# Performance work log

Measured on AMD Instinct MI355X. Metric: run time of the kernel, lower is better.

Reference implementation:

```python
import jax, jax.numpy as jnp
import numpy as np

H = 16  # heads

def setup_inputs() -> dict:
    key = jax.random.key(0)
    k1, k2, k3 = jax.random.split(key, 3)
    B, N, D = 2, 2048, 1024
    x = jax.random.normal(k1, (B, N, D), dtype=jnp.float32)
    W1 = jax.random.normal(k2, (D, 3 * D), dtype=jnp.float32) * (1.0 / np.sqrt(D))
    b1 = jnp.zeros((3 * D,), dtype=jnp.float32)
    W2 = jax.random.normal(k3, (D, D), dtype=jnp.float32) * (1.0 / np.sqrt(D))
    b2 = jnp.zeros((D,), dtype=jnp.float32)
    return {"x": x, "W1": W1, "b1": b1, "W2": W2, "b2": b2}

def reference(x, W1, b1, W2, b2):
    B, N, D = x.shape
    Dh = D // H  # head dim
    qkv = x @ W1 + b1                         # [B,N,3D]
    q, k, v = jnp.split(qkv, 3, axis=-1)
    q = q.reshape(B, N, H, Dh).transpose(0, 2, 1, 3)  # [B,H,N,Dh]
    k = k.reshape(B, N, H, Dh).transpose(0, 2, 1, 3)
    v = v.reshape(B, N, H, Dh).transpose(0, 2, 1, 3)
    scale = 1.0 / np.sqrt(Dh)
    w = jnp.einsum('bhnd,bhmd->bhnm', q, k) * scale   # [B,H,N,N]
    w = jax.nn.softmax(w, axis=-1)
    out = jnp.einsum('bhnm,bhmd->bhnd', w, v)         # [B,H,N,Dh]
    out = out.transpose(0, 2, 1, 3).reshape(B, N, D)
    return out @ W2 + b2
```

## Files before the change

kernel.cpp:

```cpp
#include <hip/hip_runtime.h>
#include <hip/hip_bf16.h>
#include <stdint.h>

#define B_   2
#define H_   16
#define N_   2048
#define D_   1024
#define DH   64
#define MTOK 4096

#define LOG2E 1.44269504088896f

typedef __attribute__((ext_vector_type(8)))  short bf16x8;
typedef __attribute__((ext_vector_type(4)))  float f32x4;
typedef __attribute__((ext_vector_type(16))) float f32x16;
typedef __attribute__((ext_vector_type(2)))  unsigned u32x2;
typedef __attribute__((ext_vector_type(4)))  unsigned short us4;

#define VMCNT_ASM(N) asm volatile("s_waitcnt vmcnt(" #N ")" ::: "memory")

static __device__ __forceinline__ unsigned short f2bf(float f) {
    union { float f; unsigned u; } v; v.f = f;
    unsigned r = v.u + 0x7fffu + ((v.u >> 16) & 1u);
    return (unsigned short)(r >> 16);
}

static __device__ __forceinline__ unsigned f2u(float x) {
    union { float f; unsigned u; } v; v.f = x; return v.u;
}
static __device__ __forceinline__ float u2f(unsigned x) {
    union { unsigned u; float f; } v; v.u = x; return v.f;
}

static __device__ __forceinline__ unsigned cvt_pk_bf16(float lo, float hi) {
    unsigned r;
    asm("v_cvt_pk_bf16_f32 %0, %1, %2" : "=v"(r) : "v"(lo), "v"(hi));
    return r;
}

static __device__ __forceinline__ bf16x8 frag_from_u32(unsigned a, unsigned b, unsigned c, unsigned d) {
    union { unsigned u[4]; bf16x8 v; } x;
    x.u[0] = a; x.u[1] = b; x.u[2] = c; x.u[3] = d;
    return x.v;
}

static __device__ __forceinline__ void load_lds16(const void* g, void* l) {
    __builtin_amdgcn_global_load_lds(
        (const __attribute__((address_space(1))) unsigned int*)g,
        (__attribute__((address_space(3))) unsigned int*)l, 16, 0, 0);
}

__global__ __launch_bounds__(256) void k_pre(const float* __restrict__ x,
                                             unsigned short* __restrict__ xb,
                                             const float* __restrict__ W1,
                                             unsigned short* __restrict__ w1t,
                                             const float* __restrict__ W2,
                                             unsigned short* __restrict__ w2t) {
    int blk = blockIdx.x;
    int t = threadIdx.x;
    if (blk < 4096) {
        int idx = (blk * 256 + t) * 4;
        float4 v = *(const float4*)(x + idx);
        us4 o;
        o.x = f2bf(v.x); o.y = f2bf(v.y); o.z = f2bf(v.z); o.w = f2bf(v.w);
        *(us4*)(xb + idx) = o;
        return;
    }
    const float* in;
    unsigned short* out;
    int C, bx, by;
    if (blk < 4864) { in = W1; out = w1t; C = 3072; int b2 = blk - 4096; bx = b2 % 48; by = b2 / 48; }
    else            { in = W2; out = w2t; C = 1024; int b2 = blk - 4864; bx = b2 % 16; by = b2 / 16; }
    const int R = 1024;
    __shared__ float tile[64][65];
    int c0 = bx * 64, r0 = by * 64;
    int tr = t >> 4, tc = (t & 15) * 4;
#pragma unroll
    for (int p = 0; p < 4; p++) {
        int row = p * 16 + tr;
        float4 v = *(const float4*)(in + (size_t)(r0 + row) * C + c0 + tc);
        tile[row][tc + 0] = v.x; tile[row][tc + 1] = v.y;
        tile[row][tc + 2] = v.z; tile[row][tc + 3] = v.w;
    }
    __syncthreads();
    int oc = t >> 4, orr = (t & 15) * 4;
#pragma unroll
    for (int p = 0; p < 4; p++) {
        int crow = p * 16 + oc;
        us4 o;
        o.x = f2bf(tile[orr + 0][crow]);
        o.y = f2bf(tile[orr + 1][crow]);
        o.z = f2bf(tile[orr + 2][crow]);
        o.w = f2bf(tile[orr + 3][crow]);
        *(us4*)(out + (size_t)(c0 + crow) * R + r0 + orr) = o;
    }
}

__global__ __launch_bounds__(512, 2) void k_gemm0(const unsigned short* __restrict__ A,
                                                  const unsigned short* __restrict__ Bt,
                                                  const float* __restrict__ bias,
                                                  unsigned short* __restrict__ qdst,
                                                  unsigned short* __restrict__ kdst,
                                                  unsigned short* __restrict__ vdst) {
    __shared__ unsigned short lds[57344];
    const int K = 1024, NT = 16;
    int tid = threadIdx.x;
    int lane = tid & 63, wv = tid >> 6;
    int wm = wv >> 2, wn = wv & 3;
    int F = blockIdx.x;
    int L = (F & 7) * 32 + (F >> 3);
    int n0 = (L % 16) * 192;
    int m0 = (L / 16) * 256;

    f32x4 acc[8][3];
#pragma unroll
    for (int i = 0; i < 8; i++)
#pragma unroll
        for (int j = 0; j < 3; j++) {
            f32x4 z; z[0] = 0.f; z[1] = 0.f; z[2] = 0.f; z[3] = 0.f;
            acc[i][j] = z;
        }

    auto stage = [&](int t) {
        int p = t & 1;
        int k0 = t * 64;
        unsigned short* ab = &lds[p * 16384];
        unsigned short* bb = &lds[32768 + p * 12288];
#pragma unroll
        for (int i = 0; i < 4; i++) {
            int u = i * 512 + tid;
            int r = u >> 3, c8 = u & 7;
            int c8s = c8 ^ (r & 7);
            int db = (i * 512 + wv * 64) * 8;
            load_lds16(A + (size_t)(m0 + r) * K + k0 + c8s * 8, &ab[db]);
            if (i < 3)
                load_lds16(Bt + (size_t)(n0 + r) * K + k0 + c8s * 8, &bb[db]);
        }
    };

    stage(0);
    stage(1);

    const int ml = lane & 15, ul = lane >> 4;
    bf16x8 afr[8], bfr[3];

#pragma unroll 1
    for (int t = 0; t < NT; ++t) {
        if (t < NT - 1) { VMCNT_ASM(7); }
        else            { VMCNT_ASM(0); }
        __builtin_amdgcn_s_barrier();

        const unsigned short* ab = &lds[(t & 1) * 16384];
        const unsigned short* bb = &lds[32768 + (t & 1) * 12288];

#pragma unroll
        for (int kk = 0; kk < 2; ++kk) {
            int ck = ((kk * 4 + ul) ^ (ml & 7)) * 8;
#pragma unroll
            for (int nj = 0; nj < 3; nj++)
                bfr[nj] = *(const bf16x8*)&bb[(wn * 48 + nj * 16 + ml) * 64 + ck];
#pragma unroll
            for (int q = 0; q < 8; q++)
                afr[q] = *(const bf16x8*)&ab[(wm * 128 + q * 16 + ml) * 64 + ck];
            __builtin_amdgcn_s_barrier();
            __builtin_amdgcn_s_setprio(1);
#pragma unroll
            for (int q = 0; q < 8; q++)
#pragma unroll
                for (int nj = 0; nj < 3; nj++)
                    acc[q][nj] = __builtin_amdgcn_mfma_f32_16x16x32_bf16(
                        afr[q], bfr[nj], acc[q][nj], 0, 0, 0);
            __builtin_amdgcn_s_setprio(0);
            __builtin_amdgcn_s_barrier();
        }
        if (t + 2 < NT) stage(t + 2);
    }

#pragma unroll
    for (int nj = 0; nj < 3; nj++) {
        int col = n0 + wn * 48 + nj * 16 + (lane & 15);
        float bv = bias[col];
        int which = col >> 10;
        int hd = (col >> 6) & 15;
        int dh = col & 63;
        float scl = (which == 0) ? (0.125f * LOG2E) : 1.0f;
#pragma unroll
        for (int mi = 0; mi < 8; mi++) {
            int rbase = m0 + wm * 128 + mi * 16 + (lane >> 4) * 4;
#pragma unroll
            for (int r = 0; r < 4; r++) {
                int tok = rbase + r;
                int bb2 = tok >> 11, nn = tok & 2047;
                float vvv = (acc[mi][nj][r] + bv) * scl;
                size_t chunk = ((size_t)(bb2 * H_ + hd) * 64 + (nn >> 5)) * 2048;
                if (which == 0) {
                    qdst[((size_t)(bb2 * H_ + hd) * N_ + nn) * DH + dh] = f2bf(vvv);
                } else if (which == 1) {
                    int lane2 = ((dh >> 3) & 1) * 32 + (nn & 31);
                    kdst[chunk + (dh >> 4) * 512 + lane2 * 8 + (dh & 7)] = f2bf(vvv);
                } else {
                    int lane2 = ((nn >> 3) & 1) * 32 + (dh & 31);
                    int islot = (dh >> 5) * 2 + ((nn >> 4) & 1);
                    vdst[chunk + islot * 512 + lane2 * 8 + (nn & 7)] = f2bf(vvv);
                }
            }
        }
    }
}

__global__ __launch_bounds__(512, 2) void k_gemm1(const unsigned short* __restrict__ A,
                                                  const unsigned short* __restrict__ Bt,
                                                  const float* __restrict__ bias,
                                                  float* __restrict__ outp) {
    __shared__ unsigned short lds1[32768];
    const int K = 1024, NT = 16;
    int tid = threadIdx.x;
    int lane = tid & 63, wv = tid >> 6;
    int wm = wv >> 2, wn = wv & 3;
    int F = blockIdx.x;
    int L = (F & 7) * 32 + (F >> 3);
    int n0 = (L % 8) * 128;
    int m0 = (L / 8) * 128;
    int bIdx = m0 >> 11;
    int ntok0 = m0 & 2047;

    f32x4 acc[4][2];
#pragma unroll
    for (int i = 0; i < 4; i++)
#pragma unroll
        for (int j = 0; j < 2; j++) {
            f32x4 z; z[0] = 0.f; z[1] = 0.f; z[2] = 0.f; z[3] = 0.f;
            acc[i][j] = z;
        }

    auto stage = [&](int t) {
        int p = t & 1;
        const unsigned short* aptr = A + ((size_t)(bIdx * H_ + t) * N_ + ntok0) * DH;
        const unsigned short* bptr = Bt + (size_t)n0 * K + t * 64;
        unsigned short* ab = &lds1[p * 8192];
        unsigned short* bb = &lds1[16384 + p * 8192];
#pragma unroll
        for (int i = 0; i < 2; i++) {
            int u = i * 512 + tid;
            int r = u >> 3, c8 = u & 7;
            int c8s = c8 ^ (r & 7);
            int db = (i * 512 + wv * 64) * 8;
            load_lds16(aptr + (size_t)r * DH + c8s * 8, &ab[db]);
            load_lds16(bptr + (size_t)r * K  + c8s * 8, &bb[db]);
        }
    };

    stage(0);
    stage(1);

    const int ml = lane & 15, ul = lane >> 4;
    bf16x8 afr[4], bfr[2];

#pragma unroll 1
    for (int t = 0; t < NT; ++t) {
        if (t < NT - 1) { VMCNT_ASM(4); }
        else            { VMCNT_ASM(0); }
        __builtin_amdgcn_s_barrier();

        const unsigned short* ab = &lds1[(t & 1) * 8192];
        const unsigned short* bb = &lds1[16384 + (t & 1) * 8192];

#pragma unroll
        for (int kk = 0; kk < 2; ++kk) {
            int ck = ((kk * 4 + ul) ^ (ml & 7)) * 8;
#pragma unroll
            for (int nj = 0; nj < 2; nj++)
                bfr[nj] = *(const bf16x8*)&bb[(wn * 32 + nj * 16 + ml) * 64 + ck];
#pragma unroll
            for (int q = 0; q < 4; q++)
                afr[q] = *(const bf16x8*)&ab[(wm * 64 + q * 16 + ml) * 64 + ck];
            __builtin_amdgcn_s_barrier();
            __builtin_amdgcn_s_setprio(1);
#pragma unroll
            for (int q = 0; q < 4; q++)
#pragma unroll
                for (int nj = 0; nj < 2; nj++)
                    acc[q][nj] = __builtin_amdgcn_mfma_f32_16x16x32_bf16(
                        afr[q], bfr[nj], acc[q][nj], 0, 0, 0);
            __builtin_amdgcn_s_setprio(0);
            __builtin_amdgcn_s_barrier();
        }
        if (t + 2 < NT) stage(t + 2);
    }

#pragma unroll
    for (int nj = 0; nj < 2; nj++) {
        int col = n0 + wn * 32 + nj * 16 + ml;
        float bv = bias[col];
#pragma unroll
        for (int mi = 0; mi < 4; mi++) {
            int rbase = m0 + wm * 64 + mi * 16 + (lane >> 4) * 4;
#pragma unroll
            for (int r = 0; r < 4; r++)
                outp[(size_t)(rbase + r) * D_ + col] = acc[mi][nj][r] + bv;
        }
    }
}

__global__ __launch_bounds__(512, 2) void k_attn(const unsigned short* __restrict__ qh,
                                                 const unsigned short* __restrict__ ks,
                                                 const unsigned short* __restrict__ vs,
                                                 unsigned short* __restrict__ o) {
    __shared__ unsigned short smem[40960];
    unsigned short* kb = smem;
    unsigned short* vb = smem + 16384;
    float* red = (float*)smem;

    int tid = threadIdx.x;
    int lane = tid & 63, wv = tid >> 6;
    int qsub = wv >> 1;
    int kvh  = wv & 1;
    int F = blockIdx.x;
    int L = (F & 7) * 64 + (F >> 3);
    int bh = L >> 4;
    int q0 = (L & 15) * 128 + qsub * 32;
    int ln = lane & 31, hi = lane >> 5;
    const size_t bhO = (size_t)bh * N_ * DH;

    const unsigned short* qp = qh + bhO;
    bf16x8 qf[4];
#pragma unroll
    for (int kk = 0; kk < 4; kk++)
        qf[kk] = *(const bf16x8*)(qp + (size_t)(q0 + ln) * DH + kk * 16 + hi * 8);

    const unsigned short* kg = ks + (size_t)bh * 131072;
    const unsigned short* vg = vs + (size_t)bh * 131072;

    int sbuf = wv >> 1;
    int sl   = wv & 1;
    int sh   = sbuf & 1;
    const unsigned short* srcb = ((sbuf >> 1) ? vg : kg) + (size_t)sh * 65536 + sl * 2048;
    auto stageT = [&](int kr, int vr, int t) {
        unsigned short* dstb = (sbuf >> 1)
            ? vb + (vr * 2 + sh) * 4096 + sl * 2048
            : kb + (kr * 2 + sh) * 4096 + sl * 2048;
#pragma unroll
        for (int i = 0; i < 4; i++)
            load_lds16(srcb + (size_t)t * 4096 + i * 512 + lane * 8, dstb + i * 512);
    };

    f32x16 o0, o1, ZEROV;
#pragma unroll
    for (int r = 0; r < 16; r++) { o0[r] = 0.f; o1[r] = 0.f; ZEROV[r] = 0.f; }
    float m = -INFINITY, l = 0.f;

    auto softmax_pv = [&](const f32x16& sa, const f32x16& sb, const unsigned short* vB) {
        float mx[8];
#pragma unroll
        for (int i = 0; i < 8; i++)
            mx[i] = fmaxf(fmaxf(sa[i], sa[i + 8]), fmaxf(sb[i], sb[i + 8]));
#pragma unroll
        for (int i = 0; i < 4; i++) mx[i] = fmaxf(mx[i], mx[i + 4]);
        float mt = fmaxf(fmaxf(mx[0], mx[2]), fmaxf(mx[1], mx[3]));
        {
            u32x2 sw = __builtin_amdgcn_permlane32_swap(f2u(mt), f2u(mt), false, false);
            mt = fmaxf(u2f(sw[0]), u2f(sw[1]));
        }
        if (!__all(mt <= m + 8.0f)) {
            float mn = fmaxf(m, mt);
            float fs = __builtin_amdgcn_exp2f(m - mn);
            m = mn;
            l *= fs;
#pragma unroll
            for (int r = 0; r < 16; r++) { o0[r] *= fs; o1[r] *= fs; }
        }
        float pa[16], pb[16];
#pragma unroll
        for (int r = 0; r < 16; r++) {
            pa[r] = __builtin_amdgcn_exp2f(sa[r] - m);
            pb[r] = __builtin_amdgcn_exp2f(sb[r] - m);
        }
        float sm[8];
#pragma unroll
        for (int i = 0; i < 8; i++) sm[i] = (pa[i] + pa[i + 8]) + (pb[i] + pb[i + 8]);
#pragma unroll
        for (int i = 0; i < 4; i++) sm[i] = sm[i] + sm[i + 4];
        float sum = (sm[0] + sm[2]) + (sm[1] + sm[3]);
        {
            u32x2 sw = __builtin_amdgcn_permlane32_swap(f2u(sum), f2u(sum), false, false);
            sum = u2f(sw[0]) + u2f(sw[1]);
        }
        l += sum;

        unsigned pka[8], pkb[8];
#pragma unroll
        for (int i = 0; i < 8; i++) {
            pka[i] = cvt_pk_bf16(pa[2 * i], pa[2 * i + 1]);
            pkb[i] = cvt_pk_bf16(pb[2 * i], pb[2 * i + 1]);
        }
        u32x2 s0 = __builtin_amdgcn_permlane32_swap(pka[0], pka[2], false, false);
        u32x2 s1 = __builtin_amdgcn_permlane32_swap(pka[1], pka[3], false, false);
        u32x2 s2 = __builtin_amdgcn_permlane32_swap(pka[4], pka[6], false, false);
        u32x2 s3 = __builtin_amdgcn_permlane32_swap(pka[5], pka[7], false, false);
        bf16x8 pf0 = frag_from_u32(s0[0], s1[0], s0[1], s1[1]);
        bf16x8 pf1 = frag_from_u32(s2[0], s3[0], s2[1], s3[1]);
        s0 = __builtin_amdgcn_permlane32_swap(pkb[0], pkb[2], false, false);
        s1 = __builtin_amdgcn_permlane32_swap(pkb[1], pkb[3], false, false);
        s2 = __builtin_amdgcn_permlane32_swap(pkb[4], pkb[6], false, false);
        s3 = __builtin_amdgcn_permlane32_swap(pkb[5], pkb[7], false, false);
        bf16x8 pf2 = frag_from_u32(s0[0], s1[0], s0[1], s1[1]);
        bf16x8 pf3 = frag_from_u32(s2[0], s3[0], s2[1], s3[1]);

        bf16x8 vf0, vf1, vf2, vf3;
        vf0 = *(const bf16x8*)&vB[0 * 512 + lane * 8];
        vf1 = *(const bf16x8*)&vB[1 * 512 + lane * 8];
        vf2 = *(const bf16x8*)&vB[2048 + 0 * 512 + lane * 8];
        vf3 = *(const bf16x8*)&vB[2048 + 1 * 512 + lane * 8];
        o0 = __builtin_amdgcn_mfma_f32_32x32x16_bf16(vf0, pf0, o0, 0, 0, 0);
        o0 = __builtin_amdgcn_mfma_f32_32x32x16_bf16(vf1, pf1, o0, 0, 0, 0);
        o0 = __builtin_amdgcn_mfma_f32_32x32x16_bf16(vf2, pf2, o0, 0, 0, 0);
        o0 = __builtin_amdgcn_mfma_f32_32x32x16_bf16(vf3, pf3, o0, 0, 0, 0);
        vf0 = *(const bf16x8*)&vB[2 * 512 + lane * 8];
        vf1 = *(const bf16x8*)&vB[3 * 512 + lane * 8];
        vf2 = *(const bf16x8*)&vB[2048 + 2 * 512 + lane * 8];
        vf3 = *(const bf16x8*)&vB[2048 + 3 * 512 + lane * 8];
        o1 = __builtin_amdgcn_mfma_f32_32x32x16_bf16(vf0, pf0, o1, 0, 0, 0);
        o1 = __builtin_amdgcn_mfma_f32_32x32x16_bf16(vf1, pf1, o1, 0, 0, 0);
        o1 = __builtin_amdgcn_mfma_f32_32x32x16_bf16(vf2, pf2, o1, 0, 0, 0);
        o1 = __builtin_amdgcn_mfma_f32_32x32x16_bf16(vf3, pf3, o1, 0, 0, 0);
    };

    stageT(0, 0, 0);
    __syncthreads();

    f32x16 sa, sb;
#pragma unroll 1
    for (int t = 0; t < 16; ++t) {
        if (t < 15) stageT((t + 1) & 1, (t + 1) % 3, t + 1);

        if (t > 0) softmax_pv(sa, sb, vb + (((t - 1) % 3) * 2 + kvh) * 4096);

        const unsigned short* kB = kb + ((t & 1) * 2 + kvh) * 4096;
        bf16x8 kfa[4], kfb[4];
#pragma unroll
        for (int i = 0; i < 4; i++) {
            kfa[i] = *(const bf16x8*)&kB[i * 512 + lane * 8];
            kfb[i] = *(const bf16x8*)&kB[2048 + i * 512 + lane * 8];
        }
        sa = __builtin_amdgcn_mfma_f32_32x32x16_bf16(kfa[0], qf[0], ZEROV, 0, 0, 0);
#pragma unroll
        for (int i = 1; i < 4; i++)
            sa = __builtin_amdgcn_mfma_f32_32x32x16_bf16(kfa[i], qf[i], sa, 0, 0, 0);
        sb = __builtin_amdgcn_mfma_f32_32x32x16_bf16(kfb[0], qf[0], ZEROV, 0, 0, 0);
#pragma unroll
        for (int i = 1; i < 4; i++)
            sb = __builtin_amdgcn_mfma_f32_32x32x16_bf16(kfb[i], qf[i], sb, 0, 0, 0);

        __syncthreads();
    }
    softmax_pv(sa, sb, vb + (0 * 2 + kvh) * 4096);
    __syncthreads();

    if (kvh == 1) {
        float* rp = red + (qsub * 64 + lane) * 34;
#pragma unroll
        for (int r = 0; r < 16; r++) { rp[r] = o0[r]; rp[16 + r] = o1[r]; }
        rp[32] = m;
        rp[33] = l;
    }
    __syncthreads();
    if (kvh == 0) {
        const float* rp = red + (qsub * 64 + lane) * 34;
        float mb = rp[32], lb = rp[33];
        float mn = fmaxf(m, mb);
        float fa = __builtin_amdgcn_exp2f(m - mn);
        float fb = __builtin_amdgcn_exp2f(mb - mn);
        float inv = 1.0f / (l * fa + lb * fb);
        float ga = fa * inv, gb = fb * inv;
        unsigned short* ob = o + bhO + (size_t)(q0 + ln) * DH;
#pragma unroll
        for (int t2 = 0; t2 < 2; t2++) {
#pragma unroll
            for (int g = 0; g < 4; g++) {
                int d = t2 * 32 + g * 8 + hi * 4;
                int rb = g * 4;
                float a0 = (t2 ? o1[rb + 0] : o0[rb + 0]) * ga + rp[t2 * 16 + rb + 0] * gb;
                float a1 = (t2 ? o1[rb + 1] : o0[rb + 1]) * ga + rp[t2 * 16 + rb + 1] * gb;
                float a2 = (t2 ? o1[rb + 2] : o0[rb + 2]) * ga + rp[t2 * 16 + rb + 2] * gb;
                float a3 = (t2 ? o1[rb + 3] : o0[rb + 3]) * ga + rp[t2 * 16 + rb + 3] * gb;
                us4 w;
                w.x = f2bf(a0); w.y = f2bf(a1); w.z = f2bf(a2); w.w = f2bf(a3);
                *(us4*)(ob + d) = w;
            }
        }
    }
}

extern "C" void kernel_launch(void* const* d_in, const int* in_sizes, int n_in,
                              void* d_out, int out_size, void* d_ws, size_t ws_size,
                              hipStream_t stream) {
    const float* x  = (const float*)d_in[0];
    const float* W1 = (const float*)d_in[1];
    const float* b1 = (const float*)d_in[2];
    const float* W2 = (const float*)d_in[3];
    const float* b2 = (const float*)d_in[4];
    float* out = (float*)d_out;

    char* ws = (char*)d_ws;
    unsigned short* xb   = (unsigned short*)(ws);
    unsigned short* w1t  = (unsigned short*)(ws + 8388608);
    unsigned short* w2t  = (unsigned short*)(ws + 14680064);
    unsigned short* qh   = (unsigned short*)(ws + 16777216);
    unsigned short* ks   = (unsigned short*)(ws + 25165824);
    unsigned short* vsb  = (unsigned short*)(ws + 33554432);
    unsigned short* attn = (unsigned short*)(ws + 41943040);

    k_pre<<<5120, 256, 0, stream>>>(x, xb, W1, w1t, W2, w2t);
    k_gemm0<<<256, 512, 0, stream>>>(xb, w1t, b1, qh, ks, vsb);
    k_attn<<<512, 512, 0, stream>>>(qh, ks, vsb, attn);
    k_gemm1<<<256, 512, 0, stream>>>(attn, w2t, b2, out);
}
```

Before: 110.1 us.

## Halve attention block to 4 waves, each wave handling two 32-row query tiles

The attention kernel now launches 256 threads per block, and each wave processes 64 query rows as two 32-row tiles. Each K/V fragment read from LDS is reused across both tiles, halving LDS traffic per unit of MFMA work. The one-tile-lagged softmax/PV software pipeline and the three-slot V ring are replaced by a simple double-buffered loop that runs QK, softmax and PV in the same iteration, with 8 loads per staging thread. Register pressure roughly doubles for the accumulators, and fewer waves per block may reduce latency hiding.

```diff
diff --git a/kernel.cpp b/kernel.cpp
--- a/kernel.cpp
+++ b/kernel.cpp
@@ -302,11 +302,11 @@
     }
 }
 
-__global__ __launch_bounds__(512, 2) void k_attn(const unsigned short* __restrict__ qh,
+__global__ __launch_bounds__(256, 2) void k_attn(const unsigned short* __restrict__ qh,
                                                  const unsigned short* __restrict__ ks,
                                                  const unsigned short* __restrict__ vs,
                                                  unsigned short* __restrict__ o) {
-    __shared__ unsigned short smem[40960];
+    __shared__ unsigned short smem[32768];
     unsigned short* kb = smem;
     unsigned short* vb = smem + 16384;
     float* red = (float*)smem;
@@ -318,38 +318,38 @@
     int F = blockIdx.x;
     int L = (F & 7) * 64 + (F >> 3);
     int bh = L >> 4;
-    int q0 = (L & 15) * 128 + qsub * 32;
+    int q0 = (L & 15) * 128 + qsub * 64;
     int ln = lane & 31, hi = lane >> 5;
     const size_t bhO = (size_t)bh * N_ * DH;
 
     const unsigned short* qp = qh + bhO;
-    bf16x8 qf[4];
-#pragma unroll
-    for (int kk = 0; kk < 4; kk++)
-        qf[kk] = *(const bf16x8*)(qp + (size_t)(q0 + ln) * DH + kk * 16 + hi * 8);
+    bf16x8 qf0[4], qf1[4];
+#pragma unroll
+    for (int kk = 0; kk < 4; kk++) {
+        qf0[kk] = *(const bf16x8*)(qp + (size_t)(q0 + ln) * DH + kk * 16 + hi * 8);
+        qf1[kk] = *(const bf16x8*)(qp + (size_t)(q0 + 32 + ln) * DH + kk * 16 + hi * 8);
+    }
 
     const unsigned short* kg = ks + (size_t)bh * 131072;
     const unsigned short* vg = vs + (size_t)bh * 131072;
 
-    int sbuf = wv >> 1;
-    int sl   = wv & 1;
-    int sh   = sbuf & 1;
-    const unsigned short* srcb = ((sbuf >> 1) ? vg : kg) + (size_t)sh * 65536 + sl * 2048;
-    auto stageT = [&](int kr, int vr, int t) {
-        unsigned short* dstb = (sbuf >> 1)
-            ? vb + (vr * 2 + sh) * 4096 + sl * 2048
-            : kb + (kr * 2 + sh) * 4096 + sl * 2048;
-#pragma unroll
-        for (int i = 0; i < 4; i++)
-            load_lds16(srcb + (size_t)t * 4096 + i * 512 + lane * 8, dstb + i * 512);
+    int sh = wv & 1;
+    unsigned short* dstb = ((wv >> 1) ? vb : kb) + sh * 8192;
+    const unsigned short* srcb = ((wv >> 1) ? vg : kg) + (size_t)sh * 65536;
+    auto stageT = [&](int ring, int t) {
+#pragma unroll
+        for (int i = 0; i < 8; i++)
+            load_lds16(srcb + (size_t)t * 4096 + i * 512 + lane * 8,
+                       dstb + ring * 4096 + i * 512);
     };
 
-    f32x16 o0, o1, ZEROV;
-#pragma unroll
-    for (int r = 0; r < 16; r++) { o0[r] = 0.f; o1[r] = 0.f; ZEROV[r] = 0.f; }
-    float m = -INFINITY, l = 0.f;
-
-    auto softmax_pv = [&](const f32x16& sa, const f32x16& sb, const unsigned short* vB) {
+    f32x16 o00, o01, o10, o11;
+#pragma unroll
+    for (int r = 0; r < 16; r++) { o00[r] = 0.f; o01[r] = 0.f; o10[r] = 0.f; o11[r] = 0.f; }
+    float m0v = -INFINITY, l0v = 0.f, m1v = -INFINITY, l1v = 0.f;
+
+    auto smax = [&](const f32x16& sa, const f32x16& sb, float& m, float& l,
+                    f32x16& oA, f32x16& oB, bf16x8* pf) {
         float mx[8];
 #pragma unroll
         for (int i = 0; i < 8; i++)
@@ -367,7 +367,7 @@
             m = mn;
             l *= fs;
 #pragma unroll
-            for (int r = 0; r < 16; r++) { o0[r] *= fs; o1[r] *= fs; }
+            for (int r = 0; r < 16; r++) { oA[r] *= fs; oB[r] *= fs; }
         }
         float pa[16], pb[16];
 #pragma unroll
@@ -397,95 +397,120 @@
         u32x2 s1 = __builtin_amdgcn_permlane32_swap(pka[1], pka[3], false, false);
         u32x2 s2 = __builtin_amdgcn_permlane32_swap(pka[4], pka[6], false, false);
         u32x2 s3 = __builtin_amdgcn_permlane32_swap(pka[5], pka[7], false, false);
-        bf16x8 pf0 = frag_from_u32(s0[0], s1[0], s0[1], s1[1]);
-        bf16x8 pf1 = frag_from_u32(s2[0], s3[0], s2[1], s3[1]);
+        pf[0] = frag_from_u32(s0[0], s1[0], s0[1], s1[1]);
+        pf[1] = frag_from_u32(s2[0], s3[0], s2[1], s3[1]);
         s0 = __builtin_amdgcn_permlane32_swap(pkb[0], pkb[2], false, false);
         s1 = __builtin_amdgcn_permlane32_swap(pkb[1], pkb[3], false, false);
         s2 = __builtin_amdgcn_permlane32_swap(pkb[4], pkb[6], false, false);
         s3 = __builtin_amdgcn_permlane32_swap(pkb[5], pkb[7], false, false);
-        bf16x8 pf2 = frag_from_u32(s0[0], s1[0], s0[1], s1[1]);
-        bf16x8 pf3 = frag_from_u32(s2[0], s3[0], s2[1], s3[1]);
-
-        bf16x8 vf0, vf1, vf2, vf3;
-        vf0 = *(const bf16x8*)&vB[0 * 512 + lane * 8];
-        vf1 = *(const bf16x8*)&vB[1 * 512 + lane * 8];
-        vf2 = *(const bf16x8*)&vB[2048 + 0 * 512 + lane * 8];
-        vf3 = *(const bf16x8*)&vB[2048 + 1 * 512 + lane * 8];
-        o0 = __builtin_amdgcn_mfma_f32_32x32x16_bf16(vf0, pf0, o0, 0, 0, 0);
-        o0 = __builtin_amdgcn_mfma_f32_32x32x16_bf16(vf1, pf1, o0, 0, 0, 0);
-        o0 = __builtin_amdgcn_mfma_f32_32x32x16_bf16(vf2, pf2, o0, 0, 0, 0);
-        o0 = __builtin_amdgcn_mfma_f32_32x32x16_bf16(vf3, pf3, o0, 0, 0, 0);
+        pf[2] = frag_from_u32(s0[0], s1[0], s0[1], s1[1]);
+        pf[3] = frag_from_u32(s2[0], s3[0], s2[1], s3[1]);
+    };
+
+    stageT(0, 0);
+    __syncthreads();
+
+#pragma unroll 1
+    for (int t = 0; t < 16; ++t) {
+        int b = t & 1;
+        if (t < 15) stageT(b ^ 1, t + 1);
+
+        const unsigned short* kB = kb + kvh * 8192 + b * 4096;
+        const unsigned short* vB = vb + kvh * 8192 + b * 4096;
+
+        bf16x8 kfa[4], kfb[4];
+#pragma unroll
+        for (int i = 0; i < 4; i++) {
+            kfa[i] = *(const bf16x8*)&kB[i * 512 + lane * 8];
+            kfb[i] = *(const bf16x8*)&kB[2048 + i * 512 + lane * 8];
+        }
+        f32x16 sa0, sb0, sa1, sb1;
+#pragma unroll
+        for (int r = 0; r < 16; r++) { sa0[r] = 0.f; sb0[r] = 0.f; sa1[r] = 0.f; sb1[r] = 0.f; }
+#pragma unroll
+        for (int i = 0; i < 4; i++) {
+            sa0 = __builtin_amdgcn_mfma_f32_32x32x16_bf16(kfa[i], qf0[i], sa0, 0, 0, 0);
+            sa1 = __builtin_amdgcn_mfma_f32_32x32x16_bf16(kfa[i], qf1[i], sa1, 0, 0, 0);
+        }
+#pragma unroll
+        for (int i = 0; i < 4; i++) {
+            sb0 = __builtin_amdgcn_mfma_f32_32x32x16_bf16(kfb[i], qf0[i], sb0, 0, 0, 0);
+            sb1 = __builtin_amdgcn_mfma_f32_32x32x16_bf16(kfb[i], qf1[i], sb1, 0, 0, 0);
+        }
+
+        bf16x8 pf0[4], pf1[4];
+        smax(sa0, sb0, m0v, l0v, o00, o01, pf0);
+        smax(sa1, sb1, m1v, l1v, o10, o11, pf1);
+
+        bf16x8 vf0 = *(const bf16x8*)&vB[0 * 512 + lane * 8];
+        bf16x8 vf1 = *(const bf16x8*)&vB[1 * 512 + lane * 8];
+        bf16x8 vf2 = *(const bf16x8*)&vB[2048 + 0 * 512 + lane * 8];
+        bf16x8 vf3 = *(const bf16x8*)&vB[2048 + 1 * 512 + lane * 8];
+        o00 = __builtin_amdgcn_mfma_f32_32x32x16_bf16(vf0, pf0[0], o00, 0, 0, 0);
+        o10 = __builtin_amdgcn_mfma_f32_32x32x16_bf16(vf0, pf1[0], o10, 0, 0, 0);
+        o00 = __builtin_amdgcn_mfma_f32_32x32x16_bf16(vf1, pf0[1], o00, 0, 0, 0);
+        o10 = __builtin_amdgcn_mfma_f32_32x32x16_bf16(vf1, pf1[1], o10, 0, 0, 0);
+        o00 = __builtin_amdgcn_mfma_f32_32x32x16_bf16(vf2, pf0[2], o00, 0, 0, 0);
+        o10 = __builtin_amdgcn_mfma_f32_32x32x16_bf16(vf2, pf1[2], o10, 0, 0, 0);
+        o00 = __builtin_amdgcn_mfma_f32_32x32x16_bf16(vf3, pf0[3], o00, 0, 0, 0);
+        o10 = __builtin_amdgcn_mfma_f32_32x32x16_bf16(vf3, pf1[3], o10, 0, 0, 0);
         vf0 = *(const bf16x8*)&vB[2 * 512 + lane * 8];
         vf1 = *(const bf16x8*)&vB[3 * 512 + lane * 8];
         vf2 = *(const bf16x8*)&vB[2048 + 2 * 512 + lane * 8];
         vf3 = *(const bf16x8*)&vB[2048 + 3 * 512 + lane * 8];
-        o1 = __builtin_amdgcn_mfma_f32_32x32x16_bf16(vf0, pf0, o1, 0, 0, 0);
-        o1 = __builtin_amdgcn_mfma_f32_32x32x16_bf16(vf1, pf1, o1, 0, 0, 0);
-        o1 = __builtin_amdgcn_mfma_f32_32x32x16_bf16(vf2, pf2, o1, 0, 0, 0);
-        o1 = __builtin_amdgcn_mfma_f32_32x32x16_bf16(vf3, pf3, o1, 0, 0, 0);
-    };
-
-    stageT(0, 0, 0);
-    __syncthreads();
-
-    f32x16 sa, sb;
-#pragma unroll 1
-    for (int t = 0; t < 16; ++t) {
-        if (t < 15) stageT((t + 1) & 1, (t + 1) % 3, t + 1);
-
-        if (t > 0) softmax_pv(sa, sb, vb + (((t - 1) % 3) * 2 + kvh) * 4096);
-
-        const unsigned short* kB = kb + ((t & 1) * 2 + kvh) * 4096;
-        bf16x8 kfa[4], kfb[4];
-#pragma unroll
-        for (int i = 0; i < 4; i++) {
-            kfa[i] = *(const bf16x8*)&kB[i * 512 + lane * 8];
-            kfb[i] = *(const bf16x8*)&kB[2048 + i * 512 + lane * 8];
-        }
-        sa = __builtin_amdgcn_mfma_f32_32x32x16_bf16(kfa[0], qf[0], ZEROV, 0, 0, 0);
-#pragma unroll
-        for (int i = 1; i < 4; i++)
-            sa = __builtin_amdgcn_mfma_f32_32x32x16_bf16(kfa[i], qf[i], sa, 0, 0, 0);
-        sb = __builtin_amdgcn_mfma_f32_32x32x16_bf16(kfb[0], qf[0], ZEROV, 0, 0, 0);
-#pragma unroll
-        for (int i = 1; i < 4; i++)
-            sb = __builtin_amdgcn_mfma_f32_32x32x16_bf16(kfb[i], qf[i], sb, 0, 0, 0);
+        o01 = __builtin_amdgcn_mfma_f32_32x32x16_bf16(vf0, pf0[0], o01, 0, 0, 0);
+        o11 = __builtin_amdgcn_mfma_f32_32x32x16_bf16(vf0, pf1[0], o11, 0, 0, 0);
+        o01 = __builtin_amdgcn_mfma_f32_32x32x16_bf16(vf1, pf0[1], o01, 0, 0, 0);
+        o11 = __builtin_amdgcn_mfma_f32_32x32x16_bf16(vf1, pf1[1], o11, 0, 0, 0);
+        o01 = __builtin_amdgcn_mfma_f32_32x32x16_bf16(vf2, pf0[2], o01, 0, 0, 0);
+        o11 = __builtin_amdgcn_mfma_f32_32x32x16_bf16(vf2, pf1[2], o11, 0, 0, 0);
+        o01 = __builtin_amdgcn_mfma_f32_32x32x16_bf16(vf3, pf0[3], o01, 0, 0, 0);
+        o11 = __builtin_amdgcn_mfma_f32_32x32x16_bf16(vf3, pf1[3], o11, 0, 0, 0);
 
         __syncthreads();
     }
-    softmax_pv(sa, sb, vb + (0 * 2 + kvh) * 4096);
-    __syncthreads();
 
     if (kvh == 1) {
-        float* rp = red + (qsub * 64 + lane) * 34;
-#pragma unroll
-        for (int r = 0; r < 16; r++) { rp[r] = o0[r]; rp[16 + r] = o1[r]; }
-        rp[32] = m;
-        rp[33] = l;
+#pragma unroll
+        for (int g = 0; g < 2; g++) {
+            float* rp = red + ((qsub * 2 + g) * 64 + lane) * 34;
+            const f32x16& oa = g ? o10 : o00;
+            const f32x16& ob2 = g ? o11 : o01;
+#pragma unroll
+            for (int r = 0; r < 16; r++) { rp[r] = oa[r]; rp[16 + r] = ob2[r]; }
+            rp[32] = g ? m1v : m0v;
+            rp[33] = g ? l1v : l0v;
+        }
     }
     __syncthreads();
     if (kvh == 0) {
-        const float* rp = red + (qsub * 64 + lane) * 34;
-        float mb = rp[32], lb = rp[33];
-        float mn = fmaxf(m, mb);
-        float fa = __builtin_amdgcn_exp2f(m - mn);
-        float fb = __builtin_amdgcn_exp2f(mb - mn);
-        float inv = 1.0f / (l * fa + lb * fb);
-        float ga = fa * inv, gb = fb * inv;
-        unsigned short* ob = o + bhO + (size_t)(q0 + ln) * DH;
-#pragma unroll
-        for (int t2 = 0; t2 < 2; t2++) {
-#pragma unroll
-            for (int g = 0; g < 4; g++) {
-                int d = t2 * 32 + g * 8 + hi * 4;
-                int rb = g * 4;
-                float a0 = (t2 ? o1[rb + 0] : o0[rb + 0]) * ga + rp[t2 * 16 + rb + 0] * gb;
-                float a1 = (t2 ? o1[rb + 1] : o0[rb + 1]) * ga + rp[t2 * 16 + rb + 1] * gb;
-                float a2 = (t2 ? o1[rb + 2] : o0[rb + 2]) * ga + rp[t2 * 16 + rb + 2] * gb;
-                float a3 = (t2 ? o1[rb + 3] : o0[rb + 3]) * ga + rp[t2 * 16 + rb + 3] * gb;
-                us4 w;
-                w.x = f2bf(a0); w.y = f2bf(a1); w.z = f2bf(a2); w.w = f2bf(a3);
-                *(us4*)(ob + d) = w;
+#pragma unroll
+        for (int g = 0; g < 2; g++) {
+            const float* rp = red + ((qsub * 2 + g) * 64 + lane) * 34;
+            float m = g ? m1v : m0v, l = g ? l1v : l0v;
+            const f32x16& oa = g ? o10 : o00;
+            const f32x16& ob2 = g ? o11 : o01;
+            float mb = rp[32], lb = rp[33];
+            float mn = fmaxf(m, mb);
+            float fa = __builtin_amdgcn_exp2f(m - mn);
+            float fb = __builtin_amdgcn_exp2f(mb - mn);
+            float inv = 1.0f / (l * fa + lb * fb);
+            float ga = fa * inv, gb = fb * inv;
+            unsigned short* ob = o + bhO + (size_t)(q0 + g * 32 + ln) * DH;
+#pragma unroll
+            for (int t2 = 0; t2 < 2; t2++) {
+#pragma unroll
+                for (int gg = 0; gg < 4; gg++) {
+                    int d = t2 * 32 + gg * 8 + hi * 4;
+                    int rb = gg * 4;
+                    float a0 = (t2 ? ob2[rb + 0] : oa[rb + 0]) * ga + rp[t2 * 16 + rb + 0] * gb;
+                    float a1 = (t2 ? ob2[rb + 1] : oa[rb + 1]) * ga + rp[t2 * 16 + rb + 1] * gb;
+                    float a2 = (t2 ? ob2[rb + 2] : oa[rb + 2]) * ga + rp[t2 * 16 + rb + 2] * gb;
+                    float a3 = (t2 ? ob2[rb + 3] : oa[rb + 3]) * ga + rp[t2 * 16 + rb + 3] * gb;
+                    us4 w;
+                    w.x = f2bf(a0); w.y = f2bf(a1); w.z = f2bf(a2); w.w = f2bf(a3);
+                    *(us4*)(ob + d) = w;
+                }
             }
         }
     }
@@ -512,6 +537,6 @@
 
     k_pre<<<5120, 256, 0, stream>>>(x, xb, W1, w1t, W2, w2t);
     k_gemm0<<<256, 512, 0, stream>>>(xb, w1t, b1, qh, ks, vsb);
-    k_attn<<<512, 512, 0, stream>>>(qh, ks, vsb, attn);
+    k_attn<<<512, 256, 0, stream>>>(qh, ks, vsb, attn);
     k_gemm1<<<256, 512, 0, stream>>>(attn, w2t, b2, out);
 }
```

New measurement: 111.8 us. No clear change (+1.5%).
